# Performance work log

Hardware: AMD Instinct MI355X
Metric: run time of the kernel (lower is better)

The kernel has to match this reference:

```python
import jax, jax.numpy as jnp
import numpy as np

B, N, D = 4, 2048, 1024
DF = 4 * D
EPS = 1e-5


def _layernorm(x, w, b):
    mu = jnp.mean(x, axis=-1, keepdims=True)
    var = jnp.mean(jnp.square(x - mu), axis=-1, keepdims=True)
    return (x - mu) * jax.lax.rsqrt(var + EPS) * w + b


def setup_inputs() -> dict:
    key = jax.random.key(0)
    ks = jax.random.split(key, 8)
    x = jax.random.normal(ks[0], (B, N, D), dtype=jnp.float32)
    # conv filter param (torch init is zeros; use small randn for numeric coverage)
    weights = jax.random.normal(ks[1], (1, 1, N), dtype=jnp.float32) * 0.02
    # registered buffer: sqrt(1/(i+1)) per token, shape (1, N, 1)
    scale = jnp.sqrt(1.0 / (jnp.arange(N, dtype=jnp.float32) + 1.0))[None, :, None]
    ln1_w = jnp.ones((D,), jnp.float32)
    ln1_b = jnp.zeros((D,), jnp.float32)
    W1 = jax.random.normal(ks[2], (DF, D), dtype=jnp.float32) * 0.02
    b1 = jnp.zeros((DF,), jnp.float32)
    W2 = jax.random.normal(ks[3], (D, DF), dtype=jnp.float32) * 0.02
    b2 = jnp.zeros((D,), jnp.float32)
    scalar = jax.random.normal(ks[4], (1,), dtype=jnp.float32) * 0.1
    ln2_w = jnp.ones((D,), jnp.float32)
    ln2_b = jnp.zeros((D,), jnp.float32)
    return dict(x=x, weights=weights, scale=scale, ln1_w=ln1_w, ln1_b=ln1_b,
                W1=W1, b1=b1, W2=W2, b2=b2, scalar=scalar, ln2_w=ln2_w, ln2_b=ln2_b)


def reference(x, weights, scale, ln1_w, ln1_b, W1, b1, W2, b2, scalar, ln2_w, ln2_b):
    n = weights.shape[-1]
    # FFT token-mixing conv: operate over token axis. x: (B,N,D) -> (B,D,N)
    xt = jnp.swapaxes(x, -2, -1)
    # real inputs -> rfft/irfft equals real(ifft(fft*fft)) from the torch code
    prod = jnp.fft.rfft(xt, n=2 * n) * jnp.fft.rfft(weights, n=2 * n)
    conv = jnp.fft.irfft(prod, n=2 * n)[..., :n]  # (B,D,N)
    x1 = jnp.swapaxes(conv, -2, -1)               # (B,N,D)
    x1 = _layernorm(x + x1 * scale, ln1_w, ln1_b)
    # GELU MLP (torch F.gelu default = exact erf gelu)
    h = jax.nn.gelu(jnp.einsum('bnd,fd->bnf', x1, W1) + b1, approximate=False)
    mlp = jnp.einsum('bnf,df->bnd', h, W2) + b2
    x2 = _layernorm(x1 + scalar * mlp, ln2_w, ln2_b)
    return x2
```

## Files before the change

### kernel.cpp

```cpp
#include <hip/hip_runtime.h>
#include <cstdint>

typedef float floatx4 __attribute__((ext_vector_type(4)));
typedef float floatx16 __attribute__((ext_vector_type(16)));
typedef int intx8 __attribute__((ext_vector_type(8)));

__device__ __forceinline__ unsigned short f2b(float f) {
  union { float f; unsigned u; } v; v.f = f;
  return (unsigned short)((v.u + 0x7FFFu + ((v.u >> 16) & 1u)) >> 16);
}
__device__ __forceinline__ float b2f(unsigned short h) {
  union { unsigned u; float f; } v; v.u = ((unsigned)h) << 16;
  return v.f;
}

__device__ __forceinline__ void gload_lds16(const void* g, void* l) {
  __builtin_amdgcn_global_load_lds(
      (const __attribute__((address_space(1))) void*)g,
      (__attribute__((address_space(3))) void*)l, 16, 0, 0);
}

__device__ __forceinline__ intx8 lds_read32s(const unsigned char* base,
                                             int lo, int hi) {
  union { intx8 v; int4 q[2]; } u;
  u.q[0] = *(const int4*)(base + lo);
  u.q[1] = *(const int4*)(base + hi);
  return u.v;
}

__device__ __forceinline__ int swz_scol(int lane) {
  return (((lane & 7) ^ ((lane >> 3) & 7)) << 4);
}

__global__ __launch_bounds__(256) void prep_kernel(
    const float* __restrict__ W1, const float* __restrict__ W2,
    const float* __restrict__ wconv, const float* __restrict__ x,
    int* __restrict__ W1f8, int* __restrict__ W2f8,
    int* __restrict__ T8, unsigned char* __restrict__ xT) {
  const int bid = blockIdx.x;
  const int tid = threadIdx.x;
  if (bid < 8192) {
    const float* in = (bid < 4096) ? W1 : W2;
    int* out = (bid < 4096) ? W1f8 : W2f8;
    long i = (long)(bid & 4095) * 256 + tid;
    float4 v = ((const float4*)in)[i];
    int pk = __builtin_amdgcn_cvt_pk_fp8_f32(v.x * 64.0f, v.y * 64.0f, 0, false);
    pk = __builtin_amdgcn_cvt_pk_fp8_f32(v.z * 64.0f, v.w * 64.0f, pk, true);
    out[i] = pk;
  } else if (bid < 12288) {
    long i = (long)(bid - 8192) * 256 + tid;
    int n = (int)(i >> 9);
    int m0 = (int)(i & 511) * 4;
    float v[4];
#pragma unroll
    for (int r = 0; r < 4; ++r) {
      int m = m0 + r;
      v[r] = (m <= n) ? wconv[n - m] * 64.0f : 0.0f;
    }
    int pk = __builtin_amdgcn_cvt_pk_fp8_f32(v[0], v[1], 0, false);
    pk = __builtin_amdgcn_cvt_pk_fp8_f32(v[2], v[3], pk, true);
    T8[i] = pk;
  } else {
    __shared__ float tile[32][33];
    const int t = bid - 12288;
    const int d0 = (t & 31) * 32;
    const int n0 = ((t >> 5) & 63) * 32;
    const int b = t >> 11;
    const int tx = tid & 31;
    const int ty = tid >> 5;
    for (int i = ty; i < 32; i += 8)
      tile[i][tx] = x[((long)b * 2048 + n0 + i) * 1024 + d0 + tx];
    __syncthreads();
    float a = tile[ty * 4 + 0][tx];
    float c = tile[ty * 4 + 1][tx];
    float e = tile[ty * 4 + 2][tx];
    float f = tile[ty * 4 + 3][tx];
    int pk = __builtin_amdgcn_cvt_pk_fp8_f32(a, c, 0, false);
    pk = __builtin_amdgcn_cvt_pk_fp8_f32(e, f, pk, true);
    *(int*)(xT + ((long)b * 1024 + d0 + tx) * 2048 + n0 + ty * 4) = pk;
  }
}

template <int EPI, int NT, bool TRI>
__global__ __launch_bounds__(256, 4) void gemm_f8(
    const unsigned char* __restrict__ A, const unsigned char* __restrict__ B,
    int Kstride, int Kloop, long zsA, long zsB, long zsC, long zsP,
    int rx, int ryb, int gxn, unsigned sclA, unsigned sclB,
    const float* __restrict__ bias,
    unsigned short* __restrict__ Cb, unsigned char* __restrict__ C8) {
  __shared__ __align__(16) unsigned char As[16 * 1040];
  __shared__ __align__(16) unsigned char Bs[16 * 1040];
  const int tid = threadIdx.x;
  const int wid = tid >> 6;
  const int lane = tid & 63;
  const int l32 = lane & 31;
  const int half = lane >> 5;
  const int wm = (wid >> 1) * 64;
  const int wn = (wid & 1) * 64;

  const int bid = blockIdx.x;
  const int xcd = bid & 7;
  const int ib = bid >> 3;
  long bm, bn;
  int kstart, kend;
  long pofs = 0;
  if (TRI) {
    const int ci = ib & 7;
    const int ri = (ib >> 3) & 1;
    const int sp = ib >> 4;
    bm = (long)(ri == 0 ? xcd : 15 - xcd) * 128;
    bn = (long)ci * 128;
    const int T = (int)(bm >> 7) + 1;
    const int h = (T + 1) >> 1;
    kstart = (sp ? h : 0) * 128;
    kend = (sp ? T : h) * 128;
    pofs = (long)sp * zsP;
  } else {
    const int ci = ib % rx;
    const int ri = ib / rx;
    const int gx = xcd % gxn;
    const int gy = xcd / gxn;
    bm = (long)(gy * ryb + ri) * 128;
    bn = (long)(gx * rx + ci) * 128;
    kstart = 0;
    kend = Kloop;
  }
  const int bz = blockIdx.z;
  const unsigned char* Ab = A + zsA * bz;
  const unsigned char* Bb = B + zsB * bz;

  floatx16 acc[2][2];
#pragma unroll
  for (int i = 0; i < 2; ++i)
#pragma unroll
    for (int j = 0; j < 2; ++j)
#pragma unroll
      for (int e = 0; e < 16; ++e) acc[i][j][e] = 0.0f;

  const int srow = tid >> 3;
  const int scol = swz_scol(lane);
  const unsigned char* gA[4];
  const unsigned char* gB[4];
  unsigned char* lA[4];
  unsigned char* lB[4];
#pragma unroll
  for (int p = 0; p < 4; ++p) {
    gA[p] = Ab + (bm + p * 32 + srow) * (long)Kstride + scol;
    gB[p] = Bb + (bn + p * 32 + srow) * (long)Kstride + scol;
    lA[p] = As + (p * 4 + wid) * 1040;
    lB[p] = Bs + (p * 4 + wid) * 1040;
  }

  int offA_lo[2][2], offA_hi[2][2], offB_lo[2][2], offB_hi[2][2];
#pragma unroll
  for (int i = 0; i < 2; ++i)
#pragma unroll
    for (int s = 0; s < 2; ++s) {
      const int q0 = s * 4 + half * 2;
      const int ra = (int)wm + i * 32 + l32;
      const int baseA = (ra >> 3) * 1040 + (ra & 7) * 128;
      offA_lo[i][s] = baseA + ((q0 ^ (ra & 7)) << 4);
      offA_hi[i][s] = baseA + (((q0 + 1) ^ (ra & 7)) << 4);
      const int rb = (int)wn + i * 32 + l32;
      const int baseB = (rb >> 3) * 1040 + (rb & 7) * 128;
      offB_lo[i][s] = baseB + ((q0 ^ (rb & 7)) << 4);
      offB_hi[i][s] = baseB + (((q0 + 1) ^ (rb & 7)) << 4);
    }

  for (int kk = kstart; kk < kend; kk += 128) {
    __syncthreads();
#pragma unroll
    for (int p = 0; p < 4; ++p) {
      gload_lds16(gA[p] + kk, lA[p]);
      gload_lds16(gB[p] + kk, lB[p]);
    }
    __syncthreads();
#pragma unroll
    for (int s = 0; s < 2; ++s) {
      intx8 b0 = lds_read32s(Bs, offB_lo[0][s], offB_hi[0][s]);
      intx8 b1 = lds_read32s(Bs, offB_lo[1][s], offB_hi[1][s]);
      intx8 a0 = lds_read32s(As, offA_lo[0][s], offA_hi[0][s]);
      intx8 a1 = lds_read32s(As, offA_lo[1][s], offA_hi[1][s]);
      acc[0][0] = __builtin_amdgcn_mfma_scale_f32_32x32x64_f8f6f4(
          a0, b0, acc[0][0], 0, 0, 0, sclA, 0, sclB);
      acc[0][1] = __builtin_amdgcn_mfma_scale_f32_32x32x64_f8f6f4(
          a0, b1, acc[0][1], 0, 0, 0, sclA, 0, sclB);
      acc[1][0] = __builtin_amdgcn_mfma_scale_f32_32x32x64_f8f6f4(
          a1, b0, acc[1][0], 0, 0, 0, sclA, 0, sclB);
      acc[1][1] = __builtin_amdgcn_mfma_scale_f32_32x32x64_f8f6f4(
          a1, b1, acc[1][1], 0, 0, 0, sclA, 0, sclB);
    }
  }

#pragma unroll
  for (int i = 0; i < 2; ++i)
#pragma unroll
    for (int j = 0; j < 2; ++j)
#pragma unroll
      for (int r = 0; r < 16; ++r) {
        long row = bm + wm + i * 32 + (r & 3) + 8 * (r >> 2) + 4 * half;
        long col = bn + wn + j * 32 + l32;
        long idx = pofs + (long)bz * zsC + row * (long)NT + col;
        float v = acc[i][j][r];
        if (EPI == 0) {
          Cb[idx] = f2b(v);
        } else {
          v += bias[col];
          float u = v * (0.7978845608f + 0.0356774081f * v * v);
          float u2 = u * u;
          float t = __fdividef(u * (15.0f + u2), 15.0f + 6.0f * u2);
          t = fminf(fmaxf(t, -1.0f), 1.0f);
          float g = 0.5f * v * (1.0f + t);
          int pk = __builtin_amdgcn_cvt_pk_fp8_f32(g, 0.0f, 0, false);
          C8[idx] = (unsigned char)(pk & 0xFF);
        }
      }
}

__global__ __launch_bounds__(256) void ln1_kernel(
    const float* __restrict__ x, const unsigned short* __restrict__ c0,
    const unsigned short* __restrict__ c1, const float* __restrict__ scale,
    const float* __restrict__ w, const float* __restrict__ b,
    unsigned short* __restrict__ outb, int* __restrict__ outf8) {
  const long row = blockIdx.x;
  const int tid = threadIdx.x;
  float4 xv = ((const float4*)x)[row * 256 + tid];
  ushort4 a4 = ((const ushort4*)c0)[row * 256 + tid];
  ushort4 e4 = ((const ushort4*)c1)[row * 256 + tid];
  const float sc = scale[row & 2047];
  float4 v;
  v.x = xv.x + sc * (b2f(a4.x) + b2f(e4.x));
  v.y = xv.y + sc * (b2f(a4.y) + b2f(e4.y));
  v.z = xv.z + sc * (b2f(a4.z) + b2f(e4.z));
  v.w = xv.w + sc * (b2f(a4.w) + b2f(e4.w));
  float s = v.x + v.y + v.z + v.w;
  float ss = v.x * v.x + v.y * v.y + v.z * v.z + v.w * v.w;
#pragma unroll
  for (int off = 32; off > 0; off >>= 1) {
    s += __shfl_down(s, off);
    ss += __shfl_down(ss, off);
  }
  __shared__ float red[8];
  const int wid = tid >> 6, lane = tid & 63;
  if (lane == 0) { red[wid] = s; red[4 + wid] = ss; }
  __syncthreads();
  s = red[0] + red[1] + red[2] + red[3];
  ss = red[4] + red[5] + red[6] + red[7];
  const float mu = s * (1.0f / 1024.0f);
  const float var = ss * (1.0f / 1024.0f) - mu * mu;
  const float rs = rsqrtf(var + 1e-5f);
  float4 wv = ((const float4*)w)[tid];
  float4 bv = ((const float4*)b)[tid];
  float o0 = (v.x - mu) * rs * wv.x + bv.x;
  float o1 = (v.y - mu) * rs * wv.y + bv.y;
  float o2 = (v.z - mu) * rs * wv.z + bv.z;
  float o3 = (v.w - mu) * rs * wv.w + bv.w;
  ushort4 u{f2b(o0), f2b(o1), f2b(o2), f2b(o3)};
  ((ushort4*)outb)[row * 256 + tid] = u;
  int pk = __builtin_amdgcn_cvt_pk_fp8_f32(o0, o1, 0, false);
  pk = __builtin_amdgcn_cvt_pk_fp8_f32(o2, o3, pk, true);
  outf8[row * 256 + tid] = pk;
}

__global__ __launch_bounds__(256) void ln2_fused_kernel(
    const unsigned short* __restrict__ y0, const unsigned short* __restrict__ y1,
    const unsigned short* __restrict__ x1b, const float* __restrict__ b2,
    const float* __restrict__ scalar_p, const float* __restrict__ w,
    const float* __restrict__ b, float* __restrict__ out) {
  const long row = blockIdx.x;
  const int tid = threadIdx.x;
  ushort4 a4 = ((const ushort4*)y0)[row * 256 + tid];
  ushort4 c4 = ((const ushort4*)y1)[row * 256 + tid];
  ushort4 xr = ((const ushort4*)x1b)[row * 256 + tid];
  float4 bias = ((const float4*)b2)[tid];
  const float scl = scalar_p[0];
  float4 v;
  v.x = b2f(xr.x) + scl * (b2f(a4.x) + b2f(c4.x) + bias.x);
  v.y = b2f(xr.y) + scl * (b2f(a4.y) + b2f(c4.y) + bias.y);
  v.z = b2f(xr.z) + scl * (b2f(a4.z) + b2f(c4.z) + bias.z);
  v.w = b2f(xr.w) + scl * (b2f(a4.w) + b2f(c4.w) + bias.w);
  float s = v.x + v.y + v.z + v.w;
  float ss = v.x * v.x + v.y * v.y + v.z * v.z + v.w * v.w;
#pragma unroll
  for (int off = 32; off > 0; off >>= 1) {
    s += __shfl_down(s, off);
    ss += __shfl_down(ss, off);
  }
  __shared__ float red[8];
  const int wid = tid >> 6, lane = tid & 63;
  if (lane == 0) { red[wid] = s; red[4 + wid] = ss; }
  __syncthreads();
  s = red[0] + red[1] + red[2] + red[3];
  ss = red[4] + red[5] + red[6] + red[7];
  const float mu = s * (1.0f / 1024.0f);
  const float var = ss * (1.0f / 1024.0f) - mu * mu;
  const float rs = rsqrtf(var + 1e-5f);
  float4 wv = ((const float4*)w)[tid];
  float4 bv = ((const float4*)b)[tid];
  float4 o;
  o.x = (v.x - mu) * rs * wv.x + bv.x;
  o.y = (v.y - mu) * rs * wv.y + bv.y;
  o.z = (v.z - mu) * rs * wv.z + bv.z;
  o.w = (v.w - mu) * rs * wv.w + bv.w;
  ((float4*)out)[row * 256 + tid] = o;
}

extern "C" void kernel_launch(void* const* d_in, const int* in_sizes, int n_in,
                              void* d_out, int out_size, void* d_ws, size_t ws_size,
                              hipStream_t stream) {
  const float* x      = (const float*)d_in[0];
  const float* wconv  = (const float*)d_in[1];
  const float* scale  = (const float*)d_in[2];
  const float* ln1w   = (const float*)d_in[3];
  const float* ln1b   = (const float*)d_in[4];
  const float* W1     = (const float*)d_in[5];
  const float* b1     = (const float*)d_in[6];
  const float* W2     = (const float*)d_in[7];
  const float* b2     = (const float*)d_in[8];
  const float* scalar = (const float*)d_in[9];
  const float* ln2w   = (const float*)d_in[10];
  const float* ln2b   = (const float*)d_in[11];
  float* out = (float*)d_out;

  const unsigned SCL_1  = 0x7F7F7F7Fu;
  const unsigned SCL_64 = 0x79797979u;

  char* ws = (char*)d_ws;
  unsigned char* xT8   = (unsigned char*)ws;  ws += (size_t)4 * 1024 * 2048;
  unsigned char* T8    = (unsigned char*)ws;  ws += (size_t)2048 * 2048;
  unsigned char* W1f8  = (unsigned char*)ws;  ws += (size_t)4096 * 1024;
  unsigned char* W2f8  = (unsigned char*)ws;  ws += (size_t)4096 * 1024;
  float* y             = (float*)ws;          ws += (size_t)8192 * 1024 * 4;
  unsigned short* yb   = (unsigned short*)ws; ws += (size_t)2 * 8192 * 1024 * 2;
  unsigned short* x1b  = (unsigned short*)ws; ws += (size_t)8192 * 1024 * 2;
  unsigned char* x1f8  = (unsigned char*)ws;  ws += (size_t)8192 * 1024;
  unsigned char* h8    = (unsigned char*)ws;  ws += (size_t)8192 * 4096;
  (void)y;

  prep_kernel<<<20480, 256, 0, stream>>>(W1, W2, wconv, x,
                                         (int*)W1f8, (int*)W2f8, (int*)T8, xT8);

  gemm_f8<0, 1024, true><<<dim3(256, 1, 4), 256, 0, stream>>>(
      T8, xT8, 2048, 2048, 0L, (long)1024 * 2048, (long)2048 * 1024,
      (long)8192 * 1024, 8, 0, 0, SCL_64, SCL_1, nullptr, yb, nullptr);
  ln1_kernel<<<8192, 256, 0, stream>>>(
      x, yb, yb + (size_t)8192 * 1024, scale, ln1w, ln1b, x1b, (int*)x1f8);
  gemm_f8<2, 4096, false><<<dim3(2048, 1, 1), 256, 0, stream>>>(
      x1f8, W1f8, 1024, 1024, 0L, 0L, 0L, 0L,
      16, 16, 2, SCL_1, SCL_64, b1, nullptr, h8);
  gemm_f8<0, 1024, false><<<dim3(512, 1, 2), 256, 0, stream>>>(
      h8, W2f8, 4096, 2048, 2048L, 2048L, (long)8192 * 1024, 0L,
      8, 8, 1, SCL_1, SCL_64, nullptr, yb, nullptr);
  ln2_fused_kernel<<<8192, 256, 0, stream>>>(
      yb, yb + (size_t)8192 * 1024, x1b, b2, scalar, ln2w, ln2b, out);
}
```

Before: 278.0 us.

## Swap MFMA operands for vectorized epilogue stores and drop LDS row padding

Swaps the A/B operands of the scaled FP8 MFMA so each lane's accumulator holds four consecutive output columns. The epilogue can then write packed ushort4 bf16 values or a packed 4-byte FP8 word instead of scalar per-element stores. It also removes the 16-byte LDS padding per 8-row group (relying on the XOR swizzle alone), which shrinks shared memory enough to raise launch bounds from 4 to 5 blocks. The risks are LDS bank conflicts without padding and more register pressure under the tighter occupancy target.

```diff
diff --git a/kernel.cpp b/kernel.cpp
--- a/kernel.cpp
+++ b/kernel.cpp
@@ -82,14 +82,14 @@
 }
 
 template <int EPI, int NT, bool TRI>
-__global__ __launch_bounds__(256, 4) void gemm_f8(
+__global__ __launch_bounds__(256, 5) void gemm_f8(
     const unsigned char* __restrict__ A, const unsigned char* __restrict__ B,
     int Kstride, int Kloop, long zsA, long zsB, long zsC, long zsP,
     int rx, int ryb, int gxn, unsigned sclA, unsigned sclB,
     const float* __restrict__ bias,
     unsigned short* __restrict__ Cb, unsigned char* __restrict__ C8) {
-  __shared__ __align__(16) unsigned char As[16 * 1040];
-  __shared__ __align__(16) unsigned char Bs[16 * 1040];
+  __shared__ __align__(16) unsigned char As[16 * 1024];
+  __shared__ __align__(16) unsigned char Bs[16 * 1024];
   const int tid = threadIdx.x;
   const int wid = tid >> 6;
   const int lane = tid & 63;
@@ -147,8 +147,8 @@
   for (int p = 0; p < 4; ++p) {
     gA[p] = Ab + (bm + p * 32 + srow) * (long)Kstride + scol;
     gB[p] = Bb + (bn + p * 32 + srow) * (long)Kstride + scol;
-    lA[p] = As + (p * 4 + wid) * 1040;
-    lB[p] = Bs + (p * 4 + wid) * 1040;
+    lA[p] = As + (p * 4 + wid) * 1024;
+    lB[p] = Bs + (p * 4 + wid) * 1024;
   }
 
   int offA_lo[2][2], offA_hi[2][2], offB_lo[2][2], offB_hi[2][2];
@@ -158,11 +158,11 @@
     for (int s = 0; s < 2; ++s) {
       const int q0 = s * 4 + half * 2;
       const int ra = (int)wm + i * 32 + l32;
-      const int baseA = (ra >> 3) * 1040 + (ra & 7) * 128;
+      const int baseA = ra * 128;
       offA_lo[i][s] = baseA + ((q0 ^ (ra & 7)) << 4);
       offA_hi[i][s] = baseA + (((q0 + 1) ^ (ra & 7)) << 4);
       const int rb = (int)wn + i * 32 + l32;
-      const int baseB = (rb >> 3) * 1040 + (rb & 7) * 128;
+      const int baseB = rb * 128;
       offB_lo[i][s] = baseB + ((q0 ^ (rb & 7)) << 4);
       offB_hi[i][s] = baseB + (((q0 + 1) ^ (rb & 7)) << 4);
     }
@@ -182,13 +182,13 @@
       intx8 a0 = lds_read32s(As, offA_lo[0][s], offA_hi[0][s]);
       intx8 a1 = lds_read32s(As, offA_lo[1][s], offA_hi[1][s]);
       acc[0][0] = __builtin_amdgcn_mfma_scale_f32_32x32x64_f8f6f4(
-          a0, b0, acc[0][0], 0, 0, 0, sclA, 0, sclB);
+          b0, a0, acc[0][0], 0, 0, 0, sclB, 0, sclA);
       acc[0][1] = __builtin_amdgcn_mfma_scale_f32_32x32x64_f8f6f4(
-          a0, b1, acc[0][1], 0, 0, 0, sclA, 0, sclB);
+          b1, a0, acc[0][1], 0, 0, 0, sclB, 0, sclA);
       acc[1][0] = __builtin_amdgcn_mfma_scale_f32_32x32x64_f8f6f4(
-          a1, b0, acc[1][0], 0, 0, 0, sclA, 0, sclB);
+          b0, a1, acc[1][0], 0, 0, 0, sclB, 0, sclA);
       acc[1][1] = __builtin_amdgcn_mfma_scale_f32_32x32x64_f8f6f4(
-          a1, b1, acc[1][1], 0, 0, 0, sclA, 0, sclB);
+          b1, a1, acc[1][1], 0, 0, 0, sclB, 0, sclA);
     }
   }
 
@@ -197,22 +197,33 @@
 #pragma unroll
     for (int j = 0; j < 2; ++j)
 #pragma unroll
-      for (int r = 0; r < 16; ++r) {
-        long row = bm + wm + i * 32 + (r & 3) + 8 * (r >> 2) + 4 * half;
-        long col = bn + wn + j * 32 + l32;
+      for (int g = 0; g < 4; ++g) {
+        long row = bm + wm + i * 32 + l32;
+        long col = bn + wn + j * 32 + 8 * g + 4 * half;
         long idx = pofs + (long)bz * zsC + row * (long)NT + col;
-        float v = acc[i][j][r];
+        float v0 = acc[i][j][g * 4 + 0];
+        float v1 = acc[i][j][g * 4 + 1];
+        float v2 = acc[i][j][g * 4 + 2];
+        float v3 = acc[i][j][g * 4 + 3];
         if (EPI == 0) {
-          Cb[idx] = f2b(v);
+          ushort4 u{f2b(v0), f2b(v1), f2b(v2), f2b(v3)};
+          *(ushort4*)(Cb + idx) = u;
         } else {
-          v += bias[col];
-          float u = v * (0.7978845608f + 0.0356774081f * v * v);
-          float u2 = u * u;
-          float t = __fdividef(u * (15.0f + u2), 15.0f + 6.0f * u2);
-          t = fminf(fmaxf(t, -1.0f), 1.0f);
-          float g = 0.5f * v * (1.0f + t);
-          int pk = __builtin_amdgcn_cvt_pk_fp8_f32(g, 0.0f, 0, false);
-          C8[idx] = (unsigned char)(pk & 0xFF);
+          float gv[4];
+          float bv[4] = {bias[col], bias[col + 1], bias[col + 2], bias[col + 3]};
+          float vv[4] = {v0, v1, v2, v3};
+#pragma unroll
+          for (int e = 0; e < 4; ++e) {
+            float v = vv[e] + bv[e];
+            float u = v * (0.7978845608f + 0.0356774081f * v * v);
+            float u2 = u * u;
+            float t = __fdividef(u * (15.0f + u2), 15.0f + 6.0f * u2);
+            t = fminf(fmaxf(t, -1.0f), 1.0f);
+            gv[e] = 0.5f * v * (1.0f + t);
+          }
+          int pk = __builtin_amdgcn_cvt_pk_fp8_f32(gv[0], gv[1], 0, false);
+          pk = __builtin_amdgcn_cvt_pk_fp8_f32(gv[2], gv[3], pk, true);
+          *(int*)(C8 + idx) = pk;
         }
       }
 }
```

Result: slower. 712.9 us (+156.4%).
